# Performance work log

Measured on AMD Instinct MI355X. Metric: run time of the kernel, lower is better.

## Reference

```python
import jax, jax.numpy as jnp
import numpy as np
import math
from jax import lax

# cfg['MODEL'] constants
MU = 0.1          # FISTA step size
LMBD = 0.1        # LAMBDA[0], sparsity weight
N_DICT = 1        # EXPANSION_FACTOR
N_STEPS = 6       # NUM_LAYERS (FISTA iterations)
K = 3             # kernel_size
PAD = 1           # padding
STRIDE = 1        # stride (POOLING=False, stride passed to conv)
DN = ('NCHW', 'OIHW', 'NCHW')


def _conv(x, w):
    # F.conv2d(x, w, stride=1, padding=PAD)
    return lax.conv_general_dilated(x, w, (STRIDE, STRIDE), [(PAD, PAD), (PAD, PAD)], dimension_numbers=DN)


def _conv_t(y, w):
    # F.conv_transpose2d(y, w, stride=1, padding=PAD) == conv2d with flipped, in/out-swapped kernel, pad K-1-PAD
    wt = jnp.transpose(jnp.flip(w, (-1, -2)), (1, 0, 2, 3))  # [Cin, Cout, K, K]
    p = K - 1 - PAD
    return lax.conv_general_dilated(y, wt, (1, 1), [(p, p), (p, p)], dimension_numbers=DN)


def _shrink(z, thr):
    # non_negative=True soft-threshold: relu(z - thr)
    return jax.nn.relu(z - thr)


def setup_inputs() -> dict:
    key = jax.random.key(0)
    k1, k2 = jax.random.split(key)
    x = jax.random.normal(k1, (16, 64, 56, 56), dtype=jnp.float32)
    # dictionary weight [out_channels, in_channels*n_dict, K, K], kaiming-ish scale
    W = jax.random.normal(k2, (128, 64 * N_DICT, K, K), dtype=jnp.float32) * 0.05
    return {"x": x, "W": W}


def reference(x, W):
    # w_norm: each output filter normalized to unit Frobenius norm
    Wn = W / jnp.sqrt(jnp.sum(W * W, axis=(1, 2, 3), keepdims=True) + 1e-12)
    thr = MU * LMBD
    xr = jnp.tile(x, (1, N_DICT, 1, 1)) if N_DICT > 1 else x

    # FISTA iteration 0: c = shrink(mu * D^T x)
    c = _shrink(MU * _conv(xr, Wn), thr)
    y = c
    c_prev = c
    t = 1.0
    for _ in range(N_STEPS - 1):
        r = xr - _conv_t(y, Wn)                       # residual x - D c
        c_new = _shrink(y + MU * _conv(r, Wn), thr)   # gradient step + shrink
        t_next = (1.0 + math.sqrt(1.0 + 4.0 * t * t)) / 2.0
        y = c_new + ((t - 1.0) / t_next) * (c_new - c_prev)  # momentum
        c_prev = c_new
        t = t_next
    # POOLING=False -> DictConv2d returns the sparse code directly
    return c_prev
```

## Files before the change

### kernel.cpp

```cpp
#include <hip/hip_runtime.h>
#include <hip/hip_bf16.h>
#include <math.h>

typedef __attribute__((ext_vector_type(8))) short short8;
typedef __attribute__((ext_vector_type(4))) float f32x4;

#define MU_  0.1f
#define THR_ 0.01f

static __device__ inline short f2bf(float f) {
    __hip_bfloat16 h = __float2bfloat16(f);
    return *reinterpret_cast<short*>(&h);
}
static __device__ inline float bf2f(unsigned short u) {
    unsigned int x = ((unsigned int)u) << 16;
    return __builtin_bit_cast(float, x);
}

#define ZB_ 5916

__global__ __launch_bounds__(256) void prep_kernel(
    const float* __restrict__ x, const float* __restrict__ W,
    float4* __restrict__ zbase, int n4,
    short* __restrict__ Xp, short* __restrict__ Wf2, short* __restrict__ Wt2) {
    __shared__ float lx[64 * 57];
    const int bid = blockIdx.x, tid = threadIdx.x;
    if (bid < ZB_) {
        int i = bid * 256 + tid;
        if (i < n4) zbase[i] = make_float4(0.f, 0.f, 0.f, 0.f);
    } else if (bid < ZB_ + 32) {
        int co = (bid - ZB_) * 4 + (tid >> 6);
        int ci = tid & 63;
        const float* wp = W + (co * 64 + ci) * 9;
        float v[9]; float s = 0.f;
#pragma unroll
        for (int t = 0; t < 9; ++t) { v[t] = wp[t]; s += v[t] * v[t]; }
#pragma unroll
        for (int off = 32; off; off >>= 1) s += __shfl_xor(s, off, 64);
        float inv = 1.0f / sqrtf(s + 1e-12f);
#pragma unroll
        for (int t = 0; t < 9; ++t) {
            Wf2[((t * 8 + (ci >> 3)) * 128 + co) * 8 + (ci & 7)] = f2bf(v[t] * inv);
            Wt2[((t * 16 + (co >> 3)) * 64 + ci) * 8 + (co & 7)] = f2bf(v[8 - t] * inv);
        }
    } else {
        int pb = bid - ZB_ - 32;
        int row = pb % 58, n = pb / 58;
        short* dst = Xp + ((size_t)(n * 58 + row) * 68) * 64;
        if (row >= 1 && row <= 56) {
            int h = row - 1;
            for (int j = tid; j < 64 * 56; j += 256) {
                int ci = j / 56, w = j - ci * 56;
                lx[ci * 57 + w] = x[((size_t)(n * 64 + ci)) * 3136 + h * 56 + w];
            }
            __syncthreads();
            for (int j = tid; j < 68 * 64; j += 256) {
                int s = j >> 6, ci = j & 63;
                float val = (s >= 2 && s < 58) ? lx[ci * 57 + (s - 2)] : 0.f;
                dst[(s << 6) + (ci ^ ((s & 7) << 3))] = f2bf(val);
            }
        } else {
            for (int j = tid; j < 68 * 64; j += 256) dst[j] = 0;
        }
    }
}

__global__ __launch_bounds__(256, 4) void conv_fwd(
    const short* __restrict__ inp,
    const short* __restrict__ Wf2,
    short* __restrict__ Yp,
    short* __restrict__ Cp,
    float* __restrict__ outp, int mode, float beta) {
    __shared__ __align__(16) short smem[14688];
    const int bid = blockIdx.x, tid = threadIdx.x;
    const int cb = bid >= 896;
    const int q = bid - cb * 896;
    const int sid = (q & 7) * 112 + (q >> 3);
    const int n = sid / 56, r = sid - n * 56 + 1;
    {
        const short8* src = (const short8*)(inp + ((size_t)(n * 58 + (r - 1)) * 68) * 64);
        for (int j = tid; j < 1632; j += 256) {
            int srow = j >> 3, w = j & 7;
            *(short8*)(smem + srow * 72 + w * 8) = src[j];
        }
    }
    const int lane = tid & 63, ct = tid >> 6, quad = lane >> 4, l15 = lane & 15;
    const int co = cb * 64 + ct * 16 + l15;
    const size_t prow = ((size_t)(n * 58 + r) * 68) * 128;

    short8 yold8[2], cold8[2];
    int pvv[2], pg[2]; bool pok[2];
#pragma unroll
    for (int k = 0; k < 2; ++k) {
        int item = tid + k * 256;
        pok[k] = item < 448;
        pvv[k] = item >> 3; pg[k] = item & 7;
        if (mode != 0 && pok[k]) {
            int s = pvv[k] + 2;
            size_t off = prow + (size_t)s * 128 + 8 * ((pg[k] + 8 * cb) ^ (s & 7));
            yold8[k] = *(const short8*)(Yp + off);
            if (mode == 1) cold8[k] = *(const short8*)(Cp + off);
        }
    }
    __syncthreads();

    f32x4 acc[4];
#pragma unroll
    for (int pt = 0; pt < 4; ++pt) acc[pt] = (f32x4){0.f, 0.f, 0.f, 0.f};

#pragma unroll
    for (int hp = 0; hp < 2; ++hp) {
        short8 Areg[9];
#pragma unroll
        for (int i = 0; i < 9; ++i) {
            int f = hp * 9 + i, t = f >> 1, half = f & 1;
            Areg[i] = *(const short8*)(Wf2 +
                ((size_t)((t * 8 + half * 4 + quad) * 128 + co)) * 8);
        }
#pragma unroll
        for (int i = 0; i < 9; ++i) {
            const int f = hp * 9 + i, t = f >> 1, half = f & 1;
            const int dh = t / 3, dw = t % 3;
            const int u = l15 + dw + 1;
            const int phys = (half * 4 + quad) ^ (u & 7);
            const int base = (dh * 68 + u) * 72 + phys * 8;
#pragma unroll
            for (int pt = 0; pt < 4; ++pt) {
                short8 bv = *(const short8*)(smem + base + pt * 1152);
                acc[pt] = __builtin_amdgcn_mfma_f32_16x16x32_bf16(Areg[i], bv, acc[pt], 0, 0, 0);
            }
        }
    }

    __syncthreads();
    short* tb_y = smem;
    short* tb_c = smem + 4608;
    if (mode != 0) {
#pragma unroll
        for (int k = 0; k < 2; ++k) if (pok[k]) {
            int o = pvv[k] * 72 + 8 * (pg[k] ^ (pvv[k] & 3));
            *(short8*)(tb_y + o) = yold8[k];
            if (mode == 1) *(short8*)(tb_c + o) = cold8[k];
        }
    }
    __syncthreads();
    const int h = r - 1;
#pragma unroll
    for (int pt = 0; pt < 4; ++pt) {
        const int px = pt * 16 + l15;
#pragma unroll
        for (int reg = 0; reg < 4; ++reg) {
            const int lch = ct * 16 + quad * 4 + reg;
            const int slot = px * 72 + (lch ^ ((px & 3) << 3));
            const float a = acc[pt][reg];
            if (mode == 0) {
                float c = fmaxf(MU_ * a - THR_, 0.f);
                short cb16 = f2bf(c);
                tb_y[slot] = cb16;
                tb_c[slot] = cb16;
            } else if (mode == 1) {
                float yold = bf2f((unsigned short)tb_y[slot]);
                float cold = bf2f((unsigned short)tb_c[slot]);
                float c = fmaxf(yold + MU_ * a - THR_, 0.f);
                tb_y[slot] = f2bf(c + beta * (c - cold));
                tb_c[slot] = f2bf(c);
            } else {
                if (px < 56) {
                    float yold = bf2f((unsigned short)tb_y[slot]);
                    float c = fmaxf(yold + MU_ * a - THR_, 0.f);
                    outp[((size_t)(n * 128 + cb * 64 + lch)) * 3136 + h * 56 + px] = c;
                }
            }
        }
    }
    if (mode != 2) {
        __syncthreads();
        for (int item = tid; item < 448; item += 256) {
            int vv = item >> 3, g = item & 7;
            int so = vv * 72 + 8 * (g ^ (vv & 3));
            short8 yv = *(const short8*)(tb_y + so);
            short8 cv = *(const short8*)(tb_c + so);
            int s = vv + 2;
            size_t off = prow + (size_t)s * 128 + 8 * ((g + 8 * cb) ^ (s & 7));
            *(short8*)(Yp + off) = yv;
            *(short8*)(Cp + off) = cv;
        }
    }
}

__global__ __launch_bounds__(256, 4) void conv_t(
    const short* __restrict__ Ypb,
    const short* __restrict__ Wt2,
    const short* __restrict__ Xp,
    short* __restrict__ Rp) {
    __shared__ __align__(16) short smem[14688];
    const int bid = blockIdx.x, tid = threadIdx.x;
    const int sid = (bid & 7) * 112 + (bid >> 3);
    const int n = sid / 56, r = sid - n * 56 + 1;
    const int lane = tid & 63, ct = tid >> 6, quad = lane >> 4, l15 = lane & 15;
    const int ci = ct * 16 + l15;
    const short8* src = (const short8*)(Ypb + ((size_t)(n * 58 + (r - 1)) * 68) * 128);
    const size_t prow = ((size_t)(n * 58 + r) * 68) * 64;

    short8 xold8[2];
    int pvv[2], pg[2]; bool pok[2];
#pragma unroll
    for (int k = 0; k < 2; ++k) {
        int item = tid + k * 256;
        pok[k] = item < 448;
        pvv[k] = item >> 3; pg[k] = item & 7;
        if (pok[k]) {
            int s = pvv[k] + 2;
            xold8[k] = *(const short8*)(Xp + prow + (size_t)s * 64 + 8 * (pg[k] ^ (s & 7)));
        }
    }

    f32x4 acc[4];
#pragma unroll
    for (int pt = 0; pt < 4; ++pt) acc[pt] = (f32x4){0.f, 0.f, 0.f, 0.f};

#pragma unroll
    for (int p = 0; p < 2; ++p) {
        if (p) __syncthreads();
        for (int j = tid; j < 1632; j += 256) {
            int srow = j >> 3, w = j & 7;
            *(short8*)(smem + srow * 72 + w * 8) = src[srow * 16 + p * 8 + w];
        }
        __syncthreads();
#pragma unroll
        for (int sub = 0; sub < 2; ++sub) {
            short8 Areg[9];
#pragma unroll
            for (int i = 0; i < 9; ++i) {
                int f = sub * 9 + i, t = f >> 1, sh = f & 1;
                Areg[i] = *(const short8*)(Wt2 +
                    ((size_t)((t * 16 + (p * 2 + sh) * 4 + quad) * 64 + ci)) * 8);
            }
#pragma unroll
            for (int i = 0; i < 9; ++i) {
                const int f = sub * 9 + i, t = f >> 1, sh = f & 1;
                const int dh = t / 3, dw = t % 3;
                const int u = l15 + dw + 1;
                const int phys = (sh * 4 + quad) ^ (u & 7);
                const int base = (dh * 68 + u) * 72 + phys * 8;
#pragma unroll
                for (int pt = 0; pt < 4; ++pt) {
                    short8 bv = *(const short8*)(smem + base + pt * 1152);
                    acc[pt] = __builtin_amdgcn_mfma_f32_16x16x32_bf16(Areg[i], bv, acc[pt], 0, 0, 0);
                }
            }
        }
    }

    __syncthreads();
    short* tb = smem;
#pragma unroll
    for (int k = 0; k < 2; ++k) if (pok[k]) {
        *(short8*)(tb + pvv[k] * 72 + 8 * (pg[k] ^ (pvv[k] & 3))) = xold8[k];
    }
    __syncthreads();
#pragma unroll
    for (int pt = 0; pt < 4; ++pt) {
        const int px = pt * 16 + l15;
#pragma unroll
        for (int reg = 0; reg < 4; ++reg) {
            const int cir = ct * 16 + quad * 4 + reg;
            const int slot = px * 72 + (cir ^ ((px & 3) << 3));
            float xo = bf2f((unsigned short)tb[slot]);
            tb[slot] = f2bf(xo - acc[pt][reg]);
        }
    }
    __syncthreads();
    for (int item = tid; item < 448; item += 256) {
        int vv = item >> 3, g = item & 7;
        short8 val = *(const short8*)(tb + vv * 72 + 8 * (g ^ (vv & 3)));
        int s = vv + 2;
        *(short8*)(Rp + prow + (size_t)s * 64 + 8 * (g ^ (s & 7))) = val;
    }
}

extern "C" void kernel_launch(void* const* d_in, const int* in_sizes, int n_in,
                              void* d_out, int out_size, void* d_ws, size_t ws_size,
                              hipStream_t stream) {
    const float* x = (const float*)d_in[0];
    const float* W = (const float*)d_in[1];
    float* out = (float*)d_out;

    const size_t XPN = (size_t)16 * 58 * 68 * 64;
    const size_t YPN = 2 * XPN;
    short* Xp = (short*)d_ws;
    short* Rp = Xp + XPN;
    short* Yp = Rp + XPN;
    short* Cp = Yp + YPN;
    short* Wf2 = Cp + YPN;
    short* Wt2 = Wf2 + 73728;

    const int n4 = (int)((XPN + YPN) * 2 / 16);
    const int prep_blocks = ZB_ + 32 + 58 * 16;
    hipLaunchKernelGGL(prep_kernel, dim3(prep_blocks), dim3(256), 0, stream,
                       x, W, (float4*)Rp, n4, Xp, Wf2, Wt2);

    dim3 b(256, 1, 1);
    hipLaunchKernelGGL(conv_fwd, dim3(1792), b, 0, stream, Xp, Wf2, Yp, Cp,
                       (float*)nullptr, 0, 0.f);
    double t = 1.0;
    for (int it = 1; it <= 5; ++it) {
        hipLaunchKernelGGL(conv_t, dim3(896), b, 0, stream, Yp, Wt2, Xp, Rp);
        double tn = (1.0 + sqrt(1.0 + 4.0 * t * t)) / 2.0;
        float beta = (float)((t - 1.0) / tn);
        hipLaunchKernelGGL(conv_fwd, dim3(1792), b, 0, stream, Rp, Wf2, Yp, Cp,
                           (it == 5) ? out : (float*)nullptr, (it == 5) ? 2 : 1,
                           beta);
        t = tn;
    }
}
```

Before: 360.5 us.

## Compute both output-channel halves per block in conv_fwd to reuse input tile

conv_fwd now has each block compute all 128 output channels for its image row, where before two blocks each computed 64 channels. This halves the grid and removes the duplicate global-to-LDS load of the input row tile. Shared memory grows to about 36KB and each thread holds twice the accumulators, which may lower occupancy and leaves fewer blocks to spread across CUs. conv_t also drops the alignment attribute on its shared array.

```diff
diff --git a/kernel.cpp b/kernel.cpp
--- a/kernel.cpp
+++ b/kernel.cpp
@@ -71,11 +71,9 @@
     short* __restrict__ Yp,
     short* __restrict__ Cp,
     float* __restrict__ outp, int mode, float beta) {
-    __shared__ __align__(16) short smem[14688];
+    __shared__ __align__(16) short smem[18432];
     const int bid = blockIdx.x, tid = threadIdx.x;
-    const int cb = bid >= 896;
-    const int q = bid - cb * 896;
-    const int sid = (q & 7) * 112 + (q >> 3);
+    const int sid = (bid & 7) * 112 + (bid >> 3);
     const int n = sid / 56, r = sid - n * 56 + 1;
     {
         const short8* src = (const short8*)(inp + ((size_t)(n * 58 + (r - 1)) * 68) * 64);
@@ -85,60 +83,67 @@
         }
     }
     const int lane = tid & 63, ct = tid >> 6, quad = lane >> 4, l15 = lane & 15;
-    const int co = cb * 64 + ct * 16 + l15;
     const size_t prow = ((size_t)(n * 58 + r) * 68) * 128;
 
-    short8 yold8[2], cold8[2];
-    int pvv[2], pg[2]; bool pok[2];
-#pragma unroll
-    for (int k = 0; k < 2; ++k) {
+    short8 yold8[4], cold8[4];
+    int pvv[4], pg[4], pcb[4]; bool pok[4];
+#pragma unroll
+    for (int k = 0; k < 4; ++k) {
         int item = tid + k * 256;
-        pok[k] = item < 448;
-        pvv[k] = item >> 3; pg[k] = item & 7;
+        pok[k] = item < 896;
+        int cbh = item >= 448;
+        int rem = item - cbh * 448;
+        pcb[k] = cbh; pvv[k] = rem >> 3; pg[k] = rem & 7;
         if (mode != 0 && pok[k]) {
             int s = pvv[k] + 2;
-            size_t off = prow + (size_t)s * 128 + 8 * ((pg[k] + 8 * cb) ^ (s & 7));
+            size_t off = prow + (size_t)s * 128 + 8 * ((pg[k] + 8 * cbh) ^ (s & 7));
             yold8[k] = *(const short8*)(Yp + off);
             if (mode == 1) cold8[k] = *(const short8*)(Cp + off);
         }
     }
     __syncthreads();
 
-    f32x4 acc[4];
-#pragma unroll
-    for (int pt = 0; pt < 4; ++pt) acc[pt] = (f32x4){0.f, 0.f, 0.f, 0.f};
-
-#pragma unroll
-    for (int hp = 0; hp < 2; ++hp) {
-        short8 Areg[9];
-#pragma unroll
-        for (int i = 0; i < 9; ++i) {
-            int f = hp * 9 + i, t = f >> 1, half = f & 1;
-            Areg[i] = *(const short8*)(Wf2 +
-                ((size_t)((t * 8 + half * 4 + quad) * 128 + co)) * 8);
-        }
-#pragma unroll
-        for (int i = 0; i < 9; ++i) {
-            const int f = hp * 9 + i, t = f >> 1, half = f & 1;
-            const int dh = t / 3, dw = t % 3;
-            const int u = l15 + dw + 1;
-            const int phys = (half * 4 + quad) ^ (u & 7);
-            const int base = (dh * 68 + u) * 72 + phys * 8;
-#pragma unroll
-            for (int pt = 0; pt < 4; ++pt) {
-                short8 bv = *(const short8*)(smem + base + pt * 1152);
-                acc[pt] = __builtin_amdgcn_mfma_f32_16x16x32_bf16(Areg[i], bv, acc[pt], 0, 0, 0);
+    f32x4 acc[2][4];
+#pragma unroll
+    for (int cbh = 0; cbh < 2; ++cbh)
+#pragma unroll
+        for (int pt = 0; pt < 4; ++pt) acc[cbh][pt] = (f32x4){0.f, 0.f, 0.f, 0.f};
+
+#pragma unroll
+    for (int cbh = 0; cbh < 2; ++cbh) {
+        const int co = cbh * 64 + ct * 16 + l15;
+#pragma unroll
+        for (int hp = 0; hp < 2; ++hp) {
+            short8 Areg[9];
+#pragma unroll
+            for (int i = 0; i < 9; ++i) {
+                int f = hp * 9 + i, t = f >> 1, half = f & 1;
+                Areg[i] = *(const short8*)(Wf2 +
+                    ((size_t)((t * 8 + half * 4 + quad) * 128 + co)) * 8);
+            }
+#pragma unroll
+            for (int i = 0; i < 9; ++i) {
+                const int f = hp * 9 + i, t = f >> 1, half = f & 1;
+                const int dh = t / 3, dw = t % 3;
+                const int u = l15 + dw + 1;
+                const int phys = (half * 4 + quad) ^ (u & 7);
+                const int base = (dh * 68 + u) * 72 + phys * 8;
+#pragma unroll
+                for (int pt = 0; pt < 4; ++pt) {
+                    short8 bv = *(const short8*)(smem + base + pt * 1152);
+                    acc[cbh][pt] = __builtin_amdgcn_mfma_f32_16x16x32_bf16(Areg[i], bv, acc[cbh][pt], 0, 0, 0);
+                }
             }
         }
     }
 
     __syncthreads();
     short* tb_y = smem;
-    short* tb_c = smem + 4608;
+    short* tb_c = smem + 9216;
     if (mode != 0) {
 #pragma unroll
-        for (int k = 0; k < 2; ++k) if (pok[k]) {
-            int o = pvv[k] * 72 + 8 * (pg[k] ^ (pvv[k] & 3));
+        for (int k = 0; k < 4; ++k) if (pok[k]) {
+            int o = pcb[k] * 4608 + pvv[k] * 72 + 8 * (pg[k] ^ (pvv[k] & 3));
             *(short8*)(tb_y + o) = yold8[k];
             if (mode == 1) *(short8*)(tb_c + o) = cold8[k];
         }
@@ -146,42 +151,45 @@
     __syncthreads();
     const int h = r - 1;
 #pragma unroll
-    for (int pt = 0; pt < 4; ++pt) {
-        const int px = pt * 16 + l15;
-#pragma unroll
-        for (int reg = 0; reg < 4; ++reg) {
-            const int lch = ct * 16 + quad * 4 + reg;
-            const int slot = px * 72 + (lch ^ ((px & 3) << 3));
-            const float a = acc[pt][reg];
-            if (mode == 0) {
-                float c = fmaxf(MU_ * a - THR_, 0.f);
-                short cb16 = f2bf(c);
-                tb_y[slot] = cb16;
-                tb_c[slot] = cb16;
-            } else if (mode == 1) {
-                float yold = bf2f((unsigned short)tb_y[slot]);
-                float cold = bf2f((unsigned short)tb_c[slot]);
-                float c = fmaxf(yold + MU_ * a - THR_, 0.f);
-                tb_y[slot] = f2bf(c + beta * (c - cold));
-                tb_c[slot] = f2bf(c);
-            } else {
-                if (px < 56) {
+    for (int cbh = 0; cbh < 2; ++cbh) {
+#pragma unroll
+        for (int pt = 0; pt < 4; ++pt) {
+            const int px = pt * 16 + l15;
+#pragma unroll
+            for (int reg = 0; reg < 4; ++reg) {
+                const int lch = ct * 16 + quad * 4 + reg;
+                const int slot = cbh * 4608 + px * 72 + (lch ^ ((px & 3) << 3));
+                const float a = acc[cbh][pt][reg];
+                if (mode == 0) {
+                    float c = fmaxf(MU_ * a - THR_, 0.f);
+                    short cb16 = f2bf(c);
+                    tb_y[slot] = cb16;
+                    tb_c[slot] = cb16;
+                } else if (mode == 1) {
                     float yold = bf2f((unsigned short)tb_y[slot]);
+                    float cold = bf2f((unsigned short)tb_c[slot]);
                     float c = fmaxf(yold + MU_ * a - THR_, 0.f);
-                    outp[((size_t)(n * 128 + cb * 64 + lch)) * 3136 + h * 56 + px] = c;
+                    tb_y[slot] = f2bf(c + beta * (c - cold));
+                    tb_c[slot] = f2bf(c);
+                } else {
+                    if (px < 56) {
+                        float yold = bf2f((unsigned short)tb_y[slot]);
+                        float c = fmaxf(yold + MU_ * a - THR_, 0.f);
+                        outp[((size_t)(n * 128 + cbh * 64 + lch)) * 3136 + h * 56 + px] = c;
+                    }
                 }
             }
         }
     }
     if (mode != 2) {
         __syncthreads();
-        for (int item = tid; item < 448; item += 256) {
-            int vv = item >> 3, g = item & 7;
-            int so = vv * 72 + 8 * (g ^ (vv & 3));
+#pragma unroll
+        for (int k = 0; k < 4; ++k) if (pok[k]) {
+            int so = pcb[k] * 4608 + pvv[k] * 72 + 8 * (pg[k] ^ (pvv[k] & 3));
             short8 yv = *(const short8*)(tb_y + so);
             short8 cv = *(const short8*)(tb_c + so);
-            int s = vv + 2;
-            size_t off = prow + (size_t)s * 128 + 8 * ((g + 8 * cb) ^ (s & 7));
+            int s = pvv[k] + 2;
+            size_t off = prow + (size_t)s * 128 + 8 * ((pg[k] + 8 * pcb[k]) ^ (s & 7));
             *(short8*)(Yp + off) = yv;
             *(short8*)(Cp + off) = cv;
         }
@@ -193,7 +201,7 @@
     const short* __restrict__ Wt2,
     const short* __restrict__ Xp,
     short* __restrict__ Rp) {
-    __shared__ __align__(16) short smem[14688];
+    __shared__ short smem[14688];
     const int bid = blockIdx.x, tid = threadIdx.x;
     const int sid = (bid & 7) * 112 + (bid >> 3);
     const int n = sid / 56, r = sid - n * 56 + 1;
@@ -301,14 +309,14 @@
                        x, W, (float4*)Rp, n4, Xp, Wf2, Wt2);
 
     dim3 b(256, 1, 1);
-    hipLaunchKernelGGL(conv_fwd, dim3(1792), b, 0, stream, Xp, Wf2, Yp, Cp,
+    hipLaunchKernelGGL(conv_fwd, dim3(896), b, 0, stream, Xp, Wf2, Yp, Cp,
                        (float*)nullptr, 0, 0.f);
     double t = 1.0;
     for (int it = 1; it <= 5; ++it) {
         hipLaunchKernelGGL(conv_t, dim3(896), b, 0, stream, Yp, Wt2, Xp, Rp);
         double tn = (1.0 + sqrt(1.0 + 4.0 * t * t)) / 2.0;
         float beta = (float)((t - 1.0) / tn);
-        hipLaunchKernelGGL(conv_fwd, dim3(1792), b, 0, stream, Rp, Wf2, Yp, Cp,
+        hipLaunchKernelGGL(conv_fwd, dim3(896), b, 0, stream, Rp, Wf2, Yp, Cp,
                            (it == 5) ? out : (float*)nullptr, (it == 5) ? 2 : 1,
                            beta);
         t = tn;
```

After: 430.5 us. 1.19x slower.
